# Kernel optimization log

Hardware: AMD Instinct MI355X
Metric: run time of the kernel (lower is better)

The kernel has to match this reference:

```python
import jax, jax.numpy as jnp
import numpy as np

B, S, D_IN, D_MODEL, H = 4, 2048, 1024, 1024, 16
HD = D_MODEL // H  # head_dim = 64


def setup_inputs() -> dict:
    key = jax.random.key(0)
    ks = jax.random.split(key, 9)
    scale = 1.0 / np.sqrt(D_IN)
    return {
        "Q": jax.random.normal(ks[0], (B, S, D_IN), jnp.float32),
        "V": jax.random.normal(ks[1], (B, S, D_IN), jnp.float32),
        "K": jax.random.normal(ks[2], (B, S, D_IN), jnp.float32),
        "wq": jax.random.uniform(ks[3], (D_IN, D_MODEL), jnp.float32, -scale, scale),
        "bq": jax.random.uniform(ks[4], (D_MODEL,), jnp.float32, -scale, scale),
        "wk": jax.random.uniform(ks[5], (D_IN, D_MODEL), jnp.float32, -scale, scale),
        "bk": jax.random.uniform(ks[6], (D_MODEL,), jnp.float32, -scale, scale),
        "wv": jax.random.uniform(ks[7], (D_IN, D_MODEL), jnp.float32, -scale, scale),
        "bv": jax.random.uniform(ks[8], (D_MODEL,), jnp.float32, -scale, scale),
    }


def _split_heads(x):
    # [B,S,D] -> [B,H,S,HD]
    return x.reshape(B, S, H, HD).transpose(0, 2, 1, 3)


def reference(Q, V, K, wq, bq, wk, bk, wv, bv):
    q = _split_heads(Q @ wq + bq)
    k = _split_heads(K @ wk + bk)
    v = _split_heads(V @ wv + bv)
    scores = jnp.einsum("bhqd,bhkd->bhqk", q, k) / jnp.sqrt(jnp.float32(HD))
    weights = jax.nn.softmax(scores, axis=-1)
    out = jnp.einsum("bhqk,bhkd->bhqd", weights, v)
    return out.transpose(0, 2, 1, 3).reshape(B, S, D_MODEL)
```

## Files before the change

kernel.cpp:

```cpp
#include <hip/hip_runtime.h>
#include <hip/hip_bf16.h>

typedef unsigned short u16;
typedef __attribute__((ext_vector_type(8))) short bf16x8;
typedef __attribute__((ext_vector_type(4))) float f32x4;
typedef __attribute__((ext_vector_type(4))) unsigned short u16x4;
typedef __attribute__((ext_vector_type(2))) unsigned u32x2;

#define NB 4
#define NS 2048
#define DIN 1024
#define DM 1024
#define NH 16
#define HD 64
#define LOG2E 1.44269504f

__device__ __forceinline__ u16 f2bf(float f) {
  union { float f; unsigned u; } x; x.f = f;
  unsigned r = x.u + 0x7fffu + ((x.u >> 16) & 1u);
  return (u16)(r >> 16);
}

__device__ __forceinline__ unsigned pk_bf16(float a, float b) {
  union { __hip_bfloat162 h; unsigned u; } cv;
  cv.h = __float22bfloat162_rn(make_float2(a, b));
  return cv.u;
}

__device__ __forceinline__ void gl_lds16(const u16* g, u16* l) {
  __builtin_amdgcn_global_load_lds((const __attribute__((address_space(1))) void*)g,
                                   (__attribute__((address_space(3))) void*)l, 16, 0, 0);
}

__global__ void cvt_kernel(const float* __restrict__ Qp, const float* __restrict__ Kp,
                           const float* __restrict__ Vp, u16* __restrict__ oq,
                           u16* __restrict__ ok, u16* __restrict__ ov, int n4) {
  const float* s = blockIdx.y == 0 ? Qp : blockIdx.y == 1 ? Kp : Vp;
  u16* d = blockIdx.y == 0 ? oq : blockIdx.y == 1 ? ok : ov;
  int stride = gridDim.x * blockDim.x;
  for (int i = blockIdx.x * blockDim.x + threadIdx.x; i < n4; i += stride) {
    f32x4 v = ((const f32x4*)s)[i];
    u16x4 o = { f2bf(v.x), f2bf(v.y), f2bf(v.z), f2bf(v.w) };
    ((u16x4*)d)[i] = o;
  }
}

__global__ void wtrans_kernel(const float* __restrict__ wqp, const float* __restrict__ wkp,
                              const float* __restrict__ wvp, u16* __restrict__ oq,
                              u16* __restrict__ ok, u16* __restrict__ ov) {
  const float* W = blockIdx.z == 0 ? wqp : blockIdx.z == 1 ? wkp : wvp;
  u16* Wt = blockIdx.z == 0 ? oq : blockIdx.z == 1 ? ok : ov;
  __shared__ float tile[64][65];
  int n0 = blockIdx.x * 64, k0 = blockIdx.y * 64;
  int t = threadIdx.x;
#pragma unroll
  for (int i = 0; i < 16; i++) {
    int idx = t + i * 256;
    int r = idx >> 6, c = idx & 63;
    tile[r][c] = W[(size_t)(k0 + r) * DM + n0 + c];
  }
  __syncthreads();
#pragma unroll
  for (int i = 0; i < 16; i++) {
    int idx = t + i * 256;
    int r = idx >> 6, c = idx & 63;
    Wt[(size_t)(n0 + r) * DIN + k0 + c] = f2bf(tile[c][r]);
  }
}

__global__ __launch_bounds__(256) void proj_kernel(
    const u16* __restrict__ Xq, const u16* __restrict__ Xk, const u16* __restrict__ Xv,
    const u16* __restrict__ Wtq, const u16* __restrict__ Wtk, const u16* __restrict__ Wtv,
    const float* __restrict__ bq, const float* __restrict__ bk, const float* __restrict__ bv,
    u16* __restrict__ oq, u16* __restrict__ ok, u16* __restrict__ ov) {
  __shared__ __align__(16) u16 Abuf[128 * 64];
  __shared__ __align__(16) u16 Bbuf[128 * 64];
  const int bid = blockIdx.x;
  const int xr = bid & 7;
  const int nt = (bid >> 3) & 7;
  const int mt = (bid >> 6) & 7;
  const int z  = bid >> 9;
  const int m0 = (mt * 8 + xr) * 128, n0 = nt * 128;
  const u16* X  = z == 0 ? Xq : z == 1 ? Xk : Xv;
  const u16* Wt = z == 0 ? Wtq : z == 1 ? Wtk : Wtv;
  const float* bias = z == 0 ? bq : z == 1 ? bk : bv;
  u16* out = z == 0 ? oq : z == 1 ? ok : ov;
  const int t = threadIdx.x, lane = t & 63, w = t >> 6;
  const int c = lane & 15, g = lane >> 4;
  const int wm = (w >> 1) * 64, wn = (w & 1) * 64;
  f32x4 acc[4][4] = {};
  for (int k0 = 0; k0 < DIN; k0 += 64) {
#pragma unroll
    for (int i = 0; i < 4; i++) {
      int idx = (w * 4 + i) * 64 + lane;
      int row = idx >> 3;
      int srck = (idx & 7) ^ (row & 7);
      gl_lds16(&X [(size_t)(m0 + row) * DIN + k0 + srck * 8], &Abuf[(w * 4 + i) * 512]);
      gl_lds16(&Wt[(size_t)(n0 + row) * DIN + k0 + srck * 8], &Bbuf[(w * 4 + i) * 512]);
    }
    __syncthreads();
#pragma unroll
    for (int ks = 0; ks < 2; ks++) {
      bf16x8 xf[4], wf[4];
      int chn = ((ks * 4 + g) ^ (c & 7)) * 8;
#pragma unroll
      for (int a = 0; a < 4; a++) {
        xf[a] = *(const bf16x8*)&Abuf[(wm + a * 16 + c) * 64 + chn];
        wf[a] = *(const bf16x8*)&Bbuf[(wn + a * 16 + c) * 64 + chn];
      }
      if (z < 2) {
#pragma unroll
        for (int i = 0; i < 4; i++)
#pragma unroll
          for (int j = 0; j < 4; j++)
            acc[i][j] = __builtin_amdgcn_mfma_f32_16x16x32_bf16(wf[i], xf[j], acc[i][j], 0, 0, 0);
      } else {
#pragma unroll
        for (int i = 0; i < 4; i++)
#pragma unroll
          for (int j = 0; j < 4; j++)
            acc[i][j] = __builtin_amdgcn_mfma_f32_16x16x32_bf16(xf[i], wf[j], acc[i][j], 0, 0, 0);
      }
    }
    __syncthreads();
  }
  if (z < 2) {
    const float sc = (z == 0) ? 0.125f * LOG2E : 1.0f;
#pragma unroll
    for (int i = 0; i < 4; i++) {
      int nb = n0 + wn + i * 16 + g * 4;
      int h = nb >> 6, d0 = nb & 63;
      f32x4 bv4 = *(const f32x4*)&bias[nb];
#pragma unroll
      for (int j = 0; j < 4; j++) {
        int mm = m0 + wm + j * 16 + c;
        int b = mm >> 11, s = mm & 2047;
        u16x4 pk;
#pragma unroll
        for (int r = 0; r < 4; r++) pk[r] = f2bf((acc[i][j][r] + bv4[r]) * sc);
        *(u16x4*)&out[((size_t)(b * NH + h) * NS + s) * HD + d0] = pk;
      }
    }
  } else {
#pragma unroll
    for (int j = 0; j < 4; j++) {
      int n = n0 + wn + j * 16 + c;
      int h = n >> 6, d = n & 63;
      float bvs = bias[n];
#pragma unroll
      for (int i = 0; i < 4; i++) {
        int mb = m0 + wm + i * 16 + g * 4;
        int b = mb >> 11, s0 = mb & 2047;
        u16x4 pk;
#pragma unroll
        for (int r = 0; r < 4; r++) pk[r] = f2bf(acc[i][j][r] + bvs);
        *(u16x4*)&out[((size_t)(b * NH + h) * HD + d) * NS + s0] = pk;
      }
    }
  }
}

__global__ __launch_bounds__(256, 2) void attn_kernel(
    const u16* __restrict__ q, const u16* __restrict__ k, const u16* __restrict__ vT,
    float* __restrict__ out) {
  __shared__ __align__(16) u16 kt[64 * 64];
  __shared__ __align__(16) u16 vt[64 * 64];
  __shared__ __align__(16) u16 pt_all[4][64 * 64];
  const int bid = blockIdx.x;
  const int xr = bid & 7;
  const int qc = (bid >> 3) & 7;
  const int h8 = bid >> 6;
  const int bh = xr + 8 * h8;
  const int t = threadIdx.x, lane = t & 63, w = t >> 6;
  const int c = lane & 15, g = lane >> 4;
  const int q0 = qc * 256 + w * 64;
  u16* pt = pt_all[w];
  const u16* qsrc = q + ((size_t)bh * NS + q0) * HD;
  const u16* ksrc = k + (size_t)bh * NS * HD;
  const u16* vsrc = vT + (size_t)bh * HD * NS;
  const int srow = lane >> 3;
  const int skc = (lane & 7) ^ srow;
  bf16x8 qf[4][2];
#pragma unroll
  for (int grp = 0; grp < 4; grp++)
#pragma unroll
    for (int ks = 0; ks < 2; ks++)
      qf[grp][ks] = *(const bf16x8*)&qsrc[(grp * 16 + c) * HD + ks * 32 + g * 8];
  bf16x8 ones;
#pragma unroll
  for (int i = 0; i < 8; i++) ones[i] = (short)0x3F80;
  f32x4 o[4][4] = {};
  f32x4 ol[4] = {};
  for (int kt0 = 0; kt0 < NS; kt0 += 64) {
#pragma unroll
    for (int j = 0; j < 2; j++) {
      int row = w * 16 + j * 8 + srow;
      gl_lds16(&ksrc[(size_t)(kt0 + row) * HD + skc * 8], &kt[(w * 16 + j * 8) * 64]);
      gl_lds16(&vsrc[(size_t)row * NS + kt0 + skc * 8], &vt[(w * 16 + j * 8) * 64]);
    }
    __syncthreads();
    bf16x8 kf[4][2], vf[4][2];
#pragma unroll
    for (int kg = 0; kg < 4; kg++)
#pragma unroll
      for (int ks = 0; ks < 2; ks++) {
        kf[kg][ks] = *(const bf16x8*)&kt[(kg * 16 + c) * 64 + (((ks * 4 + g) ^ (c & 7)) * 8)];
        vf[kg][ks] = *(const bf16x8*)&vt[(kg * 16 + c) * 64 + (((ks * 4 + g) ^ (c & 7)) * 8)];
      }
#pragma unroll
    for (int grp = 0; grp < 4; grp++) {
      f32x4 s4[4] = {};
#pragma unroll
      for (int ks = 0; ks < 2; ks++)
#pragma unroll
        for (int kg = 0; kg < 4; kg++)
          s4[kg] = __builtin_amdgcn_mfma_f32_16x16x32_bf16(kf[kg][ks], qf[grp][ks], s4[kg], 0, 0, 0);
#pragma unroll
      for (int kg = 0; kg < 4; kg++) {
        u32x2 pk;
        pk.x = pk_bf16(exp2f(s4[kg][0]), exp2f(s4[kg][1]));
        pk.y = pk_bf16(exp2f(s4[kg][2]), exp2f(s4[kg][3]));
        *(u32x2*)&pt[(grp * 16 + c) * 64 + (((kg * 2 + (g >> 1)) ^ (c & 7)) * 8) + (g & 1) * 4] = pk;
      }
    }
#pragma unroll
    for (int grp = 0; grp < 4; grp++) {
      bf16x8 pf[2];
#pragma unroll
      for (int ks = 0; ks < 2; ks++)
        pf[ks] = *(const bf16x8*)&pt[(grp * 16 + c) * 64 + (((ks * 4 + g) ^ (c & 7)) * 8)];
#pragma unroll
      for (int ks = 0; ks < 2; ks++) {
#pragma unroll
        for (int dj = 0; dj < 4; dj++)
          o[grp][dj] = __builtin_amdgcn_mfma_f32_16x16x32_bf16(vf[dj][ks], pf[ks], o[grp][dj], 0, 0, 0);
        ol[grp] = __builtin_amdgcn_mfma_f32_16x16x32_bf16(ones, pf[ks], ol[grp], 0, 0, 0);
      }
    }
    __syncthreads();
  }
  const int b = bh >> 4, h = bh & 15;
#pragma unroll
  for (int grp = 0; grp < 4; grp++) {
    float inv = 1.f / ol[grp][0];
    int s = q0 + grp * 16 + c;
#pragma unroll
    for (int dj = 0; dj < 4; dj++) {
      f32x4 ov = o[grp][dj] * inv;
      *(f32x4*)&out[((size_t)b * NS + s) * DM + h * HD + dj * 16 + g * 4] = ov;
    }
  }
}

extern "C" void kernel_launch(void* const* d_in, const int* in_sizes, int n_in,
                              void* d_out, int out_size, void* d_ws, size_t ws_size,
                              hipStream_t stream) {
  const float* Q  = (const float*)d_in[0];
  const float* V  = (const float*)d_in[1];
  const float* K  = (const float*)d_in[2];
  const float* wq = (const float*)d_in[3];
  const float* bq = (const float*)d_in[4];
  const float* wk = (const float*)d_in[5];
  const float* bk = (const float*)d_in[6];
  const float* wv = (const float*)d_in[7];
  const float* bv = (const float*)d_in[8];
  float* out = (float*)d_out;
  char* ws = (char*)d_ws;
  const size_t NX = (size_t)NB * NS * DIN;
  const size_t XB = NX * 2;
  const size_t WB = (size_t)DIN * DM * 2;
  u16* Xq   = (u16*)(ws);
  u16* Xk   = (u16*)(ws + XB);
  u16* Xv   = (u16*)(ws + 2 * XB);
  u16* Wtq  = (u16*)(ws + 3 * XB);
  u16* Wtk  = (u16*)(ws + 3 * XB + WB);
  u16* Wtv  = (u16*)(ws + 3 * XB + 2 * WB);
  u16* qws  = (u16*)(ws + 3 * XB + 3 * WB);
  u16* kws  = (u16*)(ws + 4 * XB + 3 * WB);
  u16* vTws = (u16*)(ws + 5 * XB + 3 * WB);
  const int n4 = (int)(NX / 4);
  cvt_kernel<<<dim3(1024, 3), 256, 0, stream>>>(Q, K, V, Xq, Xk, Xv, n4);
  wtrans_kernel<<<dim3(16, 16, 3), 256, 0, stream>>>(wq, wk, wv, Wtq, Wtk, Wtv);
  proj_kernel<<<1536, 256, 0, stream>>>(Xq, Xk, Xv, Wtq, Wtk, Wtv,
                                        bq, bk, bv, qws, kws, vTws);
  attn_kernel<<<512, 256, 0, stream>>>(qws, kws, vTws, out);
}
```

Measured before the change: 335.3 us.

## Halve attention query tile per wave, double grid, add MFMA priority hints

The attention kernel now gives each wave 32 query rows instead of 64 and launches 1024 blocks with a launch-bounds occupancy hint of 4. This shrinks the accumulator register set and P scratch buffer so more waves can be resident per CU. The trade-off is that K/V tiles are loaded and read from LDS twice as often per query. The change also wraps MFMA sections in s_setprio, switches to the raw hardware exp2 builtin, and uses packed bf16 conversion in the input cast kernel.

```diff
diff --git a/kernel.cpp b/kernel.cpp
--- a/kernel.cpp
+++ b/kernel.cpp
@@ -40,8 +40,10 @@
   int stride = gridDim.x * blockDim.x;
   for (int i = blockIdx.x * blockDim.x + threadIdx.x; i < n4; i += stride) {
     f32x4 v = ((const f32x4*)s)[i];
-    u16x4 o = { f2bf(v.x), f2bf(v.y), f2bf(v.z), f2bf(v.w) };
-    ((u16x4*)d)[i] = o;
+    u32x2 o;
+    o.x = pk_bf16(v.x, v.y);
+    o.y = pk_bf16(v.z, v.w);
+    ((u32x2*)d)[i] = o;
   }
 }
 
@@ -160,37 +162,38 @@
   }
 }
 
-__global__ __launch_bounds__(256, 2) void attn_kernel(
+#define NG 2
+__global__ __launch_bounds__(256, 4) void attn_kernel(
     const u16* __restrict__ q, const u16* __restrict__ k, const u16* __restrict__ vT,
     float* __restrict__ out) {
   __shared__ __align__(16) u16 kt[64 * 64];
   __shared__ __align__(16) u16 vt[64 * 64];
-  __shared__ __align__(16) u16 pt_all[4][64 * 64];
+  __shared__ __align__(16) u16 pt_all[4][NG * 16 * 64];
   const int bid = blockIdx.x;
   const int xr = bid & 7;
-  const int qc = (bid >> 3) & 7;
-  const int h8 = bid >> 6;
+  const int qc = (bid >> 3) & 15;
+  const int h8 = bid >> 7;
   const int bh = xr + 8 * h8;
   const int t = threadIdx.x, lane = t & 63, w = t >> 6;
   const int c = lane & 15, g = lane >> 4;
-  const int q0 = qc * 256 + w * 64;
+  const int q0 = qc * 128 + w * 32;
   u16* pt = pt_all[w];
   const u16* qsrc = q + ((size_t)bh * NS + q0) * HD;
   const u16* ksrc = k + (size_t)bh * NS * HD;
   const u16* vsrc = vT + (size_t)bh * HD * NS;
   const int srow = lane >> 3;
   const int skc = (lane & 7) ^ srow;
-  bf16x8 qf[4][2];
-#pragma unroll
-  for (int grp = 0; grp < 4; grp++)
+  bf16x8 qf[NG][2];
+#pragma unroll
+  for (int grp = 0; grp < NG; grp++)
 #pragma unroll
     for (int ks = 0; ks < 2; ks++)
       qf[grp][ks] = *(const bf16x8*)&qsrc[(grp * 16 + c) * HD + ks * 32 + g * 8];
   bf16x8 ones;
 #pragma unroll
   for (int i = 0; i < 8; i++) ones[i] = (short)0x3F80;
-  f32x4 o[4][4] = {};
-  f32x4 ol[4] = {};
+  f32x4 o[NG][4] = {};
+  f32x4 ol[NG] = {};
   for (int kt0 = 0; kt0 < NS; kt0 += 64) {
 #pragma unroll
     for (int j = 0; j < 2; j++) {
@@ -208,27 +211,30 @@
         vf[kg][ks] = *(const bf16x8*)&vt[(kg * 16 + c) * 64 + (((ks * 4 + g) ^ (c & 7)) * 8)];
       }
 #pragma unroll
-    for (int grp = 0; grp < 4; grp++) {
+    for (int grp = 0; grp < NG; grp++) {
       f32x4 s4[4] = {};
+      __builtin_amdgcn_s_setprio(1);
 #pragma unroll
       for (int ks = 0; ks < 2; ks++)
 #pragma unroll
         for (int kg = 0; kg < 4; kg++)
           s4[kg] = __builtin_amdgcn_mfma_f32_16x16x32_bf16(kf[kg][ks], qf[grp][ks], s4[kg], 0, 0, 0);
+      __builtin_amdgcn_s_setprio(0);
 #pragma unroll
       for (int kg = 0; kg < 4; kg++) {
         u32x2 pk;
-        pk.x = pk_bf16(exp2f(s4[kg][0]), exp2f(s4[kg][1]));
-        pk.y = pk_bf16(exp2f(s4[kg][2]), exp2f(s4[kg][3]));
+        pk.x = pk_bf16(__builtin_amdgcn_exp2f(s4[kg][0]), __builtin_amdgcn_exp2f(s4[kg][1]));
+        pk.y = pk_bf16(__builtin_amdgcn_exp2f(s4[kg][2]), __builtin_amdgcn_exp2f(s4[kg][3]));
         *(u32x2*)&pt[(grp * 16 + c) * 64 + (((kg * 2 + (g >> 1)) ^ (c & 7)) * 8) + (g & 1) * 4] = pk;
       }
     }
 #pragma unroll
-    for (int grp = 0; grp < 4; grp++) {
+    for (int grp = 0; grp < NG; grp++) {
       bf16x8 pf[2];
 #pragma unroll
       for (int ks = 0; ks < 2; ks++)
         pf[ks] = *(const bf16x8*)&pt[(grp * 16 + c) * 64 + (((ks * 4 + g) ^ (c & 7)) * 8)];
+      __builtin_amdgcn_s_setprio(1);
 #pragma unroll
       for (int ks = 0; ks < 2; ks++) {
 #pragma unroll
@@ -236,12 +242,13 @@
           o[grp][dj] = __builtin_amdgcn_mfma_f32_16x16x32_bf16(vf[dj][ks], pf[ks], o[grp][dj], 0, 0, 0);
         ol[grp] = __builtin_amdgcn_mfma_f32_16x16x32_bf16(ones, pf[ks], ol[grp], 0, 0, 0);
       }
+      __builtin_amdgcn_s_setprio(0);
     }
     __syncthreads();
   }
   const int b = bh >> 4, h = bh & 15;
 #pragma unroll
-  for (int grp = 0; grp < 4; grp++) {
+  for (int grp = 0; grp < NG; grp++) {
     float inv = 1.f / ol[grp][0];
     int s = q0 + grp * 16 + c;
 #pragma unroll
@@ -283,5 +290,5 @@
   wtrans_kernel<<<dim3(16, 16, 3), 256, 0, stream>>>(wq, wk, wv, Wtq, Wtk, Wtv);
   proj_kernel<<<1536, 256, 0, stream>>>(Xq, Xk, Xv, Wtq, Wtk, Wtv,
                                         bq, bk, bv, qws, kws, vTws);
-  attn_kernel<<<512, 256, 0, stream>>>(qws, kws, vTws, out);
-}
+  attn_kernel<<<1024, 256, 0, stream>>>(qws, kws, vTws, out);
+}
```

New measurement: 478.0 us. +42.6%, slower.
